# Kernel tuning notes

Hardware: AMD Instinct MI355X
Metric: run time of the kernel (lower is better)

## Reference

```python
import jax, jax.numpy as jnp
import numpy as np


def _gcn_layer(x, W, b, src, dst, norm, n_nodes):
    # x: [N, Fin]; transform first (PyG GCNConv): h = x @ W
    h = x @ W  # [N, Fout]
    # gather-scale-scatter: out[d] += norm_e * h[s] over edges (incl. self loops)
    msgs = h[src] * norm[:, None]  # [E+N, Fout]
    agg = jax.ops.segment_sum(msgs, dst, num_segments=n_nodes)
    return agg + b


def setup_inputs() -> dict:
    key = jax.random.key(0)
    k1, k2, k3, k4 = jax.random.split(key, 4)
    N, E, F_IN, HID, OUT = 50000, 800000, 128, 256, 128
    x = jax.random.normal(k1, (N, F_IN), dtype=jnp.float32)
    edge_index = jax.random.randint(k2, (2, E), 0, N, dtype=jnp.int64)
    W1 = jax.random.normal(k3, (F_IN, HID), dtype=jnp.float32) / np.sqrt(F_IN)
    b1 = jnp.zeros((HID,), dtype=jnp.float32)
    W2 = jax.random.normal(k4, (HID, OUT), dtype=jnp.float32) / np.sqrt(HID)
    b2 = jnp.zeros((OUT,), dtype=jnp.float32)
    return {"x": x, "edge_index": edge_index, "W1": W1, "b1": b1, "W2": W2, "b2": b2}


def reference(x, edge_index, W1, b1, W2, b2):
    N = x.shape[0]
    # GCN normalization with self loops: A_hat = D^-1/2 (A + I) D^-1/2
    self_loops = jnp.arange(N, dtype=edge_index.dtype)
    src = jnp.concatenate([edge_index[0], self_loops])
    dst = jnp.concatenate([edge_index[1], self_loops])
    deg = jax.ops.segment_sum(jnp.ones_like(dst, dtype=x.dtype), dst, num_segments=N)
    dinv = jnp.where(deg > 0, jax.lax.rsqrt(deg), 0.0)
    norm = dinv[src] * dinv[dst]  # [E+N]
    h = _gcn_layer(x, W1, b1, src, dst, norm, N)
    h = jax.nn.relu(h)  # dropout is identity in eval mode
    out = _gcn_layer(h, W2, b2, src, dst, norm, N)
    return out  # unsupervised mode returns raw embeddings [N, 128]
```

## Files before the change

kernel.cpp:

```cpp
#include <hip/hip_runtime.h>
#include <hip/hip_bf16.h>


static constexpr int N_NODES = 50000;
static constexpr int N_EDGES = 800000;
static constexpr int F_IN = 128;
static constexpr int HID  = 256;
static constexpr int F_OUT = 128;
static constexpr int H2P  = HID + 8;

typedef __attribute__((ext_vector_type(8))) short short8;
typedef __attribute__((ext_vector_type(4))) float f32x4;

__device__ __forceinline__ unsigned short f2bf(float f) {
    union { float f; unsigned u; } x; x.f = f;
    unsigned r = x.u + 0x7FFF + ((x.u >> 16) & 1);
    return (unsigned short)(r >> 16);
}
__device__ __forceinline__ float bf2f(unsigned short h) {
    union { unsigned u; float f; } x; x.u = ((unsigned)h) << 16;
    return x.f;
}

__global__ void deg_wt_kernel(const int* __restrict__ dst, int* __restrict__ deg,
                              int* __restrict__ pos, int E,
                              const float* __restrict__ W1, unsigned short* __restrict__ w1t,
                              const float* __restrict__ W2, unsigned short* __restrict__ w2t,
                              int EB, int NB1) {
    const int b = blockIdx.x;
    if (b < EB) {
        int i = b * 256 + threadIdx.x;
        if (i < E) pos[i] = atomicAdd(&deg[dst[i]], 1);
    } else if (b < EB + NB1) {
        int t = (b - EB) * 256 + threadIdx.x;
        if (t < F_IN * HID) {
            int n = t / F_IN, k = t - n * F_IN;
            w1t[t] = f2bf(W1[(size_t)k * HID + n]);
        }
    } else {
        int t = (b - EB - NB1) * 256 + threadIdx.x;
        if (t < HID * F_OUT) {
            int n = t / HID, k = t - n * HID;
            w2t[t] = f2bf(W2[(size_t)k * F_OUT + n]);
        }
    }
}

__global__ __launch_bounds__(256) void scan_reduce_dinv(const int* __restrict__ deg,
                                                        int* __restrict__ bsums,
                                                        float* __restrict__ dinv, int N) {
    int i = blockIdx.x * 256 + threadIdx.x;
    int v = (i < N) ? deg[i] : 0;
    if (i < N) dinv[i] = rsqrtf((float)(v + 1));
#pragma unroll
    for (int ofs = 32; ofs > 0; ofs >>= 1) v += __shfl_down(v, ofs);
    __shared__ int ws[4];
    if ((threadIdx.x & 63) == 0) ws[threadIdx.x >> 6] = v;
    __syncthreads();
    if (threadIdx.x == 0) bsums[blockIdx.x] = ws[0] + ws[1] + ws[2] + ws[3];
}

__global__ __launch_bounds__(256) void scan_final_scalex(const int* __restrict__ deg,
                                                         const int* __restrict__ bsums,
                                                         int* __restrict__ off, int N, int nb,
                                                         const float* __restrict__ x,
                                                         const float* __restrict__ dinv,
                                                         unsigned short* __restrict__ xs) {
    const int tid = threadIdx.x;
    if ((int)blockIdx.x >= nb) {
        int i = (blockIdx.x - nb) * 256 + tid;
        if (i < N_NODES * F_IN / 8) {
            float dv = dinv[i >> 4];
            float4 v0 = ((const float4*)x)[i * 2];
            float4 v1 = ((const float4*)x)[i * 2 + 1];
            short8 o;
            o[0] = (short)f2bf(v0.x * dv); o[1] = (short)f2bf(v0.y * dv);
            o[2] = (short)f2bf(v0.z * dv); o[3] = (short)f2bf(v0.w * dv);
            o[4] = (short)f2bf(v1.x * dv); o[5] = (short)f2bf(v1.y * dv);
            o[6] = (short)f2bf(v1.z * dv); o[7] = (short)f2bf(v1.w * dv);
            *(short8*)(xs + (size_t)i * 8) = o;
        }
        return;
    }
    __shared__ int bs[256];
    __shared__ int s[256];
    bs[tid] = (tid < nb) ? bsums[tid] : 0;
    const int i = blockIdx.x * 256 + tid;
    int v = (i < N) ? deg[i] : 0;
    s[tid] = v;
    __syncthreads();
    for (int ofs = 1; ofs < 256; ofs <<= 1) {
        int tb = (tid >= ofs) ? bs[tid - ofs] : 0;
        int tv = (tid >= ofs) ? s[tid - ofs] : 0;
        __syncthreads();
        bs[tid] += tb;
        s[tid] += tv;
        __syncthreads();
    }
    int bbase = (blockIdx.x == 0) ? 0 : bs[blockIdx.x - 1];
    int excl = (tid == 0) ? 0 : s[tid - 1];
    if (i <= N) off[i] = bbase + excl;
}

__global__ void scatter_kernel(const int* __restrict__ src, const int* __restrict__ dst,
                               const int* __restrict__ pos, const int* __restrict__ off,
                               int* __restrict__ csr, int E) {
    int i = blockIdx.x * blockDim.x + threadIdx.x;
    if (i < E) csr[off[dst[i]] + pos[i]] = src[i];
}

template <int MODE>
__global__ __launch_bounds__(256) void agg_bf16(const unsigned short* __restrict__ hs,
                                                const int* __restrict__ off,
                                                const int* __restrict__ csr,
                                                const float* __restrict__ dinv,
                                                const float* __restrict__ bias,
                                                void* __restrict__ outp, int N) {
    const int wid = threadIdx.x >> 6;
    const int n = blockIdx.x * 4 + wid;
    if (n >= N) return;
    const int lane = threadIdx.x & 63;
    const int lane16 = lane & 15;
    const int slot = lane >> 4;

    float va[8], vb[8], vc[8], vd[8];
#pragma unroll
    for (int j = 0; j < 8; j++) { va[j] = 0.f; vb[j] = 0.f; vc[j] = 0.f; vd[j] = 0.f; }

    if (slot == 0) {
        short8 s = *(const short8*)(hs + (size_t)n * 128 + lane16 * 8);
#pragma unroll
        for (int j = 0; j < 8; j++) va[j] = bf2f((unsigned short)s[j]);
    }

    const int e0 = off[n];
    const int e1 = off[n + 1];
    for (int e = e0 + slot; e < e1; e += 16) {
        const int i1 = e + 4, i2 = e + 8, i3 = e + 12;
        const float f1 = (i1 < e1) ? 1.f : 0.f;
        const float f2 = (i2 < e1) ? 1.f : 0.f;
        const float f3 = (i3 < e1) ? 1.f : 0.f;
        const int c1 = min(i1, e1 - 1), c2 = min(i2, e1 - 1), c3 = min(i3, e1 - 1);
        int s0 = csr[e];
        int s1 = csr[c1];
        int s2 = csr[c2];
        int s3 = csr[c3];
        short8 v0 = *(const short8*)(hs + (size_t)s0 * 128 + lane16 * 8);
        short8 v1 = *(const short8*)(hs + (size_t)s1 * 128 + lane16 * 8);
        short8 v2 = *(const short8*)(hs + (size_t)s2 * 128 + lane16 * 8);
        short8 v3 = *(const short8*)(hs + (size_t)s3 * 128 + lane16 * 8);
#pragma unroll
        for (int j = 0; j < 8; j++) va[j] += bf2f((unsigned short)v0[j]);
#pragma unroll
        for (int j = 0; j < 8; j++) vb[j] = fmaf(f1, bf2f((unsigned short)v1[j]), vb[j]);
#pragma unroll
        for (int j = 0; j < 8; j++) vc[j] = fmaf(f2, bf2f((unsigned short)v2[j]), vc[j]);
#pragma unroll
        for (int j = 0; j < 8; j++) vd[j] = fmaf(f3, bf2f((unsigned short)v3[j]), vd[j]);
    }
#pragma unroll
    for (int j = 0; j < 8; j++) va[j] += vb[j] + vc[j] + vd[j];

#pragma unroll
    for (int j = 0; j < 8; j++) va[j] += __shfl_down(va[j], 32);
#pragma unroll
    for (int j = 0; j < 8; j++) va[j] += __shfl_down(va[j], 16);

    if (lane < 16) {
        float dv = dinv[n];
        if (MODE == 0) {
            short8 o;
#pragma unroll
            for (int j = 0; j < 8; j++) o[j] = (short)f2bf(va[j] * dv);
            *(short8*)((unsigned short*)outp + (size_t)n * 128 + lane * 8) = o;
        } else {
            float* op = (float*)outp + (size_t)n * 128 + lane * 8;
            float4 o0, o1;
            o0.x = va[0] * dv + bias[lane * 8 + 0];
            o0.y = va[1] * dv + bias[lane * 8 + 1];
            o0.z = va[2] * dv + bias[lane * 8 + 2];
            o0.w = va[3] * dv + bias[lane * 8 + 3];
            o1.x = va[4] * dv + bias[lane * 8 + 4];
            o1.y = va[5] * dv + bias[lane * 8 + 5];
            o1.z = va[6] * dv + bias[lane * 8 + 6];
            o1.w = va[7] * dv + bias[lane * 8 + 7];
            ((float4*)op)[0] = o0;
            ((float4*)op)[1] = o1;
        }
    }
}

__global__ __launch_bounds__(256) void gemm12(const unsigned short* __restrict__ Y,
                                              const unsigned short* __restrict__ w1t,
                                              const float* __restrict__ b1,
                                              const unsigned short* __restrict__ w2t,
                                              const float* __restrict__ dinv,
                                              unsigned short* __restrict__ hs2, int M) {
    __shared__ unsigned short h2s[64 * H2P];

    const int wid = threadIdx.x >> 6;
    const int lane = threadIdx.x & 63;
    const int an = lane & 15;
    const int q = lane >> 4;
    const int rowgrp = wid & 1;
    const int colgrp = wid >> 1;
    const int m0 = blockIdx.x * 64 + rowgrp * 32;
    const int lrow0 = rowgrp * 32;

    {
        short8 a[2][4];
#pragma unroll
        for (int r = 0; r < 2; r++) {
            int row = m0 + r * 16 + an;
            if (row >= M) row = M - 1;
            const unsigned short* xp = Y + (size_t)row * F_IN + q * 8;
#pragma unroll
            for (int c = 0; c < 4; c++) a[r][c] = *(const short8*)(xp + c * 32);
        }
#pragma unroll 4
        for (int t = 0; t < 8; t++) {
            const int col = (colgrp * 8 + t) * 16 + an;
            const unsigned short* wp = w1t + (size_t)col * F_IN + q * 8;
            short8 b[4];
#pragma unroll
            for (int c = 0; c < 4; c++) b[c] = *(const short8*)(wp + c * 32);
            f32x4 acc0 = {0.f, 0.f, 0.f, 0.f};
            f32x4 acc1 = {0.f, 0.f, 0.f, 0.f};
#pragma unroll
            for (int c = 0; c < 4; c++) {
                acc0 = __builtin_amdgcn_mfma_f32_16x16x32_bf16(a[0][c], b[c], acc0, 0, 0, 0);
                acc1 = __builtin_amdgcn_mfma_f32_16x16x32_bf16(a[1][c], b[c], acc1, 0, 0, 0);
            }
            const float bv = b1[col];
#pragma unroll
            for (int rr = 0; rr < 4; rr++) {
                h2s[(lrow0 + q * 4 + rr) * H2P + col]      = f2bf(fmaxf(acc0[rr] + bv, 0.f));
                h2s[(lrow0 + 16 + q * 4 + rr) * H2P + col] = f2bf(fmaxf(acc1[rr] + bv, 0.f));
            }
        }
    }
    __syncthreads();

    {
        short8 a[2][8];
#pragma unroll
        for (int r = 0; r < 2; r++) {
            const unsigned short* hp = &h2s[(lrow0 + r * 16 + an) * H2P + q * 8];
#pragma unroll
            for (int c = 0; c < 8; c++) a[r][c] = *(const short8*)(hp + c * 32);
        }
#pragma unroll 2
        for (int t = 0; t < 4; t++) {
            const int col = (colgrp * 4 + t) * 16 + an;
            const unsigned short* wp = w2t + (size_t)col * HID + q * 8;
            short8 b[8];
#pragma unroll
            for (int c = 0; c < 8; c++) b[c] = *(const short8*)(wp + c * 32);
            f32x4 acc0 = {0.f, 0.f, 0.f, 0.f};
            f32x4 acc1 = {0.f, 0.f, 0.f, 0.f};
#pragma unroll
            for (int c = 0; c < 8; c++) {
                acc0 = __builtin_amdgcn_mfma_f32_16x16x32_bf16(a[0][c], b[c], acc0, 0, 0, 0);
                acc1 = __builtin_amdgcn_mfma_f32_16x16x32_bf16(a[1][c], b[c], acc1, 0, 0, 0);
            }
#pragma unroll
            for (int rr = 0; rr < 4; rr++) {
                int m = m0 + q * 4 + rr;
                if (m < M) hs2[(size_t)m * F_OUT + col] = f2bf(acc0[rr] * dinv[m]);
                int m2 = m0 + 16 + q * 4 + rr;
                if (m2 < M) hs2[(size_t)m2 * F_OUT + col] = f2bf(acc1[rr] * dinv[m2]);
            }
        }
    }
}

extern "C" void kernel_launch(void* const* d_in, const int* in_sizes, int n_in,
                              void* d_out, int out_size, void* d_ws, size_t ws_size,
                              hipStream_t stream) {
    const float* x  = (const float*)d_in[0];
    const int*   ei = (const int*)d_in[1];
    const float* W1 = (const float*)d_in[2];
    const float* b1 = (const float*)d_in[3];
    const float* W2 = (const float*)d_in[4];
    const float* b2 = (const float*)d_in[5];

    const int N = N_NODES;
    const int E = N_EDGES;
    const int* srcp = ei;
    const int* dstp = ei + E;

    char* base = (char*)d_ws;
    size_t o = 0;
    auto alloc = [&](size_t bytes) {
        void* p = base + o;
        o = (o + bytes + 255) & ~(size_t)255;
        return p;
    };
    int*            deg  = (int*)alloc((size_t)N * 4);
    int*            offs = (int*)alloc((size_t)(N + 1) * 4);
    float*          dinv = (float*)alloc((size_t)N * 4);
    int*            bsum = (int*)alloc(256 * 4);
    int*            pos  = (int*)alloc((size_t)E * 4);
    int*            csr  = (int*)alloc((size_t)E * 4);
    unsigned short* xs   = (unsigned short*)alloc((size_t)N * F_IN * 2);
    unsigned short* Y    = (unsigned short*)alloc((size_t)N * F_IN * 2);
    unsigned short* w1t  = (unsigned short*)alloc((size_t)F_IN * HID * 2);
    unsigned short* w2t  = (unsigned short*)alloc((size_t)HID * F_OUT * 2);
    unsigned short* hs2  = xs;

    hipMemsetAsync(deg, 0, (size_t)N * 4, stream);

    const int NB  = (N + 256) / 256;
    const int NBX = (N * F_IN / 8 + 255) / 256;
    const int EB  = (E + 255) / 256;
    const int NB1 = (F_IN * HID + 255) / 256;
    const int NB2 = (HID * F_OUT + 255) / 256;

    deg_wt_kernel<<<EB + NB1 + NB2, 256, 0, stream>>>(dstp, deg, pos, E, W1, w1t, W2, w2t, EB, NB1);
    scan_reduce_dinv<<<NB, 256, 0, stream>>>(deg, bsum, dinv, N);
    scan_final_scalex<<<NB + NBX, 256, 0, stream>>>(deg, bsum, offs, N, NB, x, dinv, xs);
    scatter_kernel<<<EB, 256, 0, stream>>>(srcp, dstp, pos, offs, csr, E);

    agg_bf16<0><<<(N + 3) / 4, 256, 0, stream>>>(xs, offs, csr, dinv, nullptr, Y, N);
    gemm12<<<(N + 63) / 64, 256, 0, stream>>>(Y, w1t, b1, w2t, dinv, hs2, N);
    agg_bf16<1><<<(N + 3) / 4, 256, 0, stream>>>(hs2, offs, csr, dinv, b2, d_out, N);
}
```

Measured before the change: 251.6 us.

## Split fused two-layer GEMM into separate weight-resident GEMM kernels

Replaces the fused gemm12 kernel, which kept the hidden activations in shared memory, with a templated GEMM run twice. Each wave keeps its slice of the weight matrix in registers and loops over several 16-row tiles, so weights are loaded once per wave instead of once per column tile. The cost is writing and re-reading a bf16 N×256 hidden buffer in global memory, plus an extra kernel launch. Register pressure from the resident weight fragments may reduce occupancy.

```diff
diff --git a/kernel.cpp b/kernel.cpp
--- a/kernel.cpp
+++ b/kernel.cpp
@@ -7,7 +7,6 @@
 static constexpr int F_IN = 128;
 static constexpr int HID  = 256;
 static constexpr int F_OUT = 128;
-static constexpr int H2P  = HID + 8;
 
 typedef __attribute__((ext_vector_type(8))) short short8;
 typedef __attribute__((ext_vector_type(4))) float f32x4;
@@ -190,85 +189,62 @@
     }
 }
 
-__global__ __launch_bounds__(256) void gemm12(const unsigned short* __restrict__ Y,
-                                              const unsigned short* __restrict__ w1t,
-                                              const float* __restrict__ b1,
-                                              const unsigned short* __restrict__ w2t,
-                                              const float* __restrict__ dinv,
-                                              unsigned short* __restrict__ hs2, int M) {
-    __shared__ unsigned short h2s[64 * H2P];
-
+template <int K, int NC, int CPW, int EPI, int TPB>
+__global__ __launch_bounds__(256) void gemm_bres(const unsigned short* __restrict__ X,
+                                                 const unsigned short* __restrict__ WT,
+                                                 const float* __restrict__ bias,
+                                                 const float* __restrict__ dinv,
+                                                 unsigned short* __restrict__ out, int M) {
+    constexpr int KC = K / 32;
+    constexpr int CT = CPW / 16;
     const int wid = threadIdx.x >> 6;
     const int lane = threadIdx.x & 63;
     const int an = lane & 15;
     const int q = lane >> 4;
-    const int rowgrp = wid & 1;
-    const int colgrp = wid >> 1;
-    const int m0 = blockIdx.x * 64 + rowgrp * 32;
-    const int lrow0 = rowgrp * 32;
-
-    {
-        short8 a[2][4];
-#pragma unroll
-        for (int r = 0; r < 2; r++) {
-            int row = m0 + r * 16 + an;
-            if (row >= M) row = M - 1;
-            const unsigned short* xp = Y + (size_t)row * F_IN + q * 8;
-#pragma unroll
-            for (int c = 0; c < 4; c++) a[r][c] = *(const short8*)(xp + c * 32);
-        }
-#pragma unroll 4
-        for (int t = 0; t < 8; t++) {
-            const int col = (colgrp * 8 + t) * 16 + an;
-            const unsigned short* wp = w1t + (size_t)col * F_IN + q * 8;
-            short8 b[4];
-#pragma unroll
-            for (int c = 0; c < 4; c++) b[c] = *(const short8*)(wp + c * 32);
-            f32x4 acc0 = {0.f, 0.f, 0.f, 0.f};
-            f32x4 acc1 = {0.f, 0.f, 0.f, 0.f};
-#pragma unroll
-            for (int c = 0; c < 4; c++) {
-                acc0 = __builtin_amdgcn_mfma_f32_16x16x32_bf16(a[0][c], b[c], acc0, 0, 0, 0);
-                acc1 = __builtin_amdgcn_mfma_f32_16x16x32_bf16(a[1][c], b[c], acc1, 0, 0, 0);
-            }
-            const float bv = b1[col];
+    const int col0 = wid * CPW;
+
+    short8 b[CT][KC];
+    float bv[CT];
+#pragma unroll
+    for (int t = 0; t < CT; t++) {
+        const int col = col0 + t * 16 + an;
+        const unsigned short* wp = WT + (size_t)col * K + q * 8;
+#pragma unroll
+        for (int c = 0; c < KC; c++) b[t][c] = *(const short8*)(wp + c * 32);
+        if (EPI == 1) bv[t] = bias[col];
+    }
+
+    const int rt0 = blockIdx.x * TPB;
+#pragma unroll
+    for (int it = 0; it < TPB; it++) {
+        const int r0 = (rt0 + it) * 16;
+        if (r0 >= M) break;
+        int arow = r0 + an;
+        if (arow >= M) arow = M - 1;
+        const unsigned short* xp = X + (size_t)arow * K + q * 8;
+        short8 a[KC];
+#pragma unroll
+        for (int c = 0; c < KC; c++) a[c] = *(const short8*)(xp + c * 32);
+
+        float4 dv4;
+        if (EPI == 0) dv4 = *(const float4*)&dinv[r0 + q * 4];
+
+#pragma unroll
+        for (int t = 0; t < CT; t++) {
+            f32x4 acc = {0.f, 0.f, 0.f, 0.f};
+#pragma unroll
+            for (int c = 0; c < KC; c++)
+                acc = __builtin_amdgcn_mfma_f32_16x16x32_bf16(a[c], b[t][c], acc, 0, 0, 0);
+            const int col = col0 + t * 16 + an;
 #pragma unroll
             for (int rr = 0; rr < 4; rr++) {
-                h2s[(lrow0 + q * 4 + rr) * H2P + col]      = f2bf(fmaxf(acc0[rr] + bv, 0.f));
-                h2s[(lrow0 + 16 + q * 4 + rr) * H2P + col] = f2bf(fmaxf(acc1[rr] + bv, 0.f));
-            }
-        }
-    }
-    __syncthreads();
-
-    {
-        short8 a[2][8];
-#pragma unroll
-        for (int r = 0; r < 2; r++) {
-            const unsigned short* hp = &h2s[(lrow0 + r * 16 + an) * H2P + q * 8];
-#pragma unroll
-            for (int c = 0; c < 8; c++) a[r][c] = *(const short8*)(hp + c * 32);
-        }
-#pragma unroll 2
-        for (int t = 0; t < 4; t++) {
-            const int col = (colgrp * 4 + t) * 16 + an;
-            const unsigned short* wp = w2t + (size_t)col * HID + q * 8;
-            short8 b[8];
-#pragma unroll
-            for (int c = 0; c < 8; c++) b[c] = *(const short8*)(wp + c * 32);
-            f32x4 acc0 = {0.f, 0.f, 0.f, 0.f};
-            f32x4 acc1 = {0.f, 0.f, 0.f, 0.f};
-#pragma unroll
-            for (int c = 0; c < 8; c++) {
-                acc0 = __builtin_amdgcn_mfma_f32_16x16x32_bf16(a[0][c], b[c], acc0, 0, 0, 0);
-                acc1 = __builtin_amdgcn_mfma_f32_16x16x32_bf16(a[1][c], b[c], acc1, 0, 0, 0);
-            }
-#pragma unroll
-            for (int rr = 0; rr < 4; rr++) {
-                int m = m0 + q * 4 + rr;
-                if (m < M) hs2[(size_t)m * F_OUT + col] = f2bf(acc0[rr] * dinv[m]);
-                int m2 = m0 + 16 + q * 4 + rr;
-                if (m2 < M) hs2[(size_t)m2 * F_OUT + col] = f2bf(acc1[rr] * dinv[m2]);
+                const int m = r0 + q * 4 + rr;
+                if (m < M) {
+                    float v = acc[rr];
+                    if (EPI == 1) v = fmaxf(v + bv[t], 0.f);
+                    else v *= ((const float*)&dv4)[rr];
+                    out[(size_t)m * NC + col] = f2bf(v);
+                }
             }
         }
     }
@@ -304,6 +280,7 @@
     int*            csr  = (int*)alloc((size_t)E * 4);
     unsigned short* xs   = (unsigned short*)alloc((size_t)N * F_IN * 2);
     unsigned short* Y    = (unsigned short*)alloc((size_t)N * F_IN * 2);
+    unsigned short* h2   = (unsigned short*)alloc((size_t)N * HID * 2);
     unsigned short* w1t  = (unsigned short*)alloc((size_t)F_IN * HID * 2);
     unsigned short* w2t  = (unsigned short*)alloc((size_t)HID * F_OUT * 2);
     unsigned short* hs2  = xs;
@@ -322,6 +299,10 @@
     scatter_kernel<<<EB, 256, 0, stream>>>(srcp, dstp, pos, offs, csr, E);
 
     agg_bf16<0><<<(N + 3) / 4, 256, 0, stream>>>(xs, offs, csr, dinv, nullptr, Y, N);
-    gemm12<<<(N + 63) / 64, 256, 0, stream>>>(Y, w1t, b1, w2t, dinv, hs2, N);
+
+    const int NT16 = (N + 15) / 16;
+    gemm_bres<F_IN, HID, 64, 1, 4><<<(NT16 + 3) / 4, 256, 0, stream>>>(Y, w1t, b1, nullptr, h2, N);
+    gemm_bres<HID, F_OUT, 32, 0, 4><<<(NT16 + 3) / 4, 256, 0, stream>>>(h2, w2t, nullptr, dinv, hs2, N);
+
     agg_bf16<1><<<(N + 3) / 4, 256, 0, stream>>>(hs2, offs, csr, dinv, b2, d_out, N);
 }
```

New measurement: 260.0 us. 1.03x slower.
